# Performance work log

Measured on AMD Instinct MI355X. Metric: run time of the kernel, lower is better.

Reference implementation:

```python
import jax, jax.numpy as jnp
import numpy as np

K = 8          # kernels per group
H = 32         # groups (g // divisor)
NUM_DIL = 14   # int(log2((75000-1)/8)) + 1


def _gconv1d(x, w, d, p):
    # x: (B, H, T), w: (H*K, 1, 9) grouped conv, dilation d, padding p
    return jax.lax.conv_general_dilated(
        x, w, window_strides=(1,), padding=[(p, p)], rhs_dilation=(d,),
        dimension_numbers=("NCH", "OIH", "NCH"), feature_group_count=H)


def setup_inputs() -> dict:
    key = jax.random.key(0)
    kX, kW, kI = jax.random.split(key, 3)
    X = jax.random.normal(kX, (4, 17, 75000), dtype=jnp.float32)
    W = jax.random.normal(kW, (NUM_DIL, 2, K * H, 1, 9), dtype=jnp.float32)
    W = W - W.mean(-1, keepdims=True)
    W = W / jnp.abs(W).sum(-1, keepdims=True)
    idx = jax.random.randint(kI, (NUM_DIL, 2, H, 8), 0, 17, dtype=jnp.int32)
    return {"X": X, "W": W, "idx": idx}


def reference(X, W, idx):
    B = X.shape[0]
    diff_X = jnp.diff(X, axis=-1)  # (B, C, T-1)
    bi = jnp.arange(B)[:, None, None]
    hi = jnp.arange(H)[None, :, None]
    outs = []
    for di in range(NUM_DIL):
        d = 2 ** di
        p = 4 * d  # (9-1)*d // 2
        for diff_i in range(2):
            src = X if diff_i == 0 else diff_X
            # channel gather + sum: (B, H, 8, T) -> (B, H, T)
            g = src[:, idx[di, diff_i]].sum(2)
            z = _gconv1d(g, W[di, diff_i], d, p)  # (B, H*K, L)
            z = z.reshape(B, H, K, -1)            # (B, H, K, L)
            max_v = z.max(2)                       # (B, H, L)
            max_i = z.argmax(2)
            min_i = z.argmin(2)
            count_max = jnp.zeros((B, H, K), z.dtype).at[bi, hi, max_i].add(max_v)
            count_min = jnp.zeros((B, H, K), z.dtype).at[bi, hi, min_i].add(1.0)
            outs.append(count_max)
            outs.append(count_min)
    return jnp.concatenate(outs, axis=1).reshape(B, -1)  # (B, 14336)
```

## Files before the change

kernel.cpp:

```cpp
#include <hip/hip_runtime.h>

typedef float F2 __attribute__((ext_vector_type(2)));

#define NB 4
#define NC 17
#define T0 75000
#define NH 32
#define NK 8

__global__ void diffK(const float* __restrict__ X, float* __restrict__ D) {
    int t = blockIdx.x * 256 + threadIdx.x;
    int row = blockIdx.y;
    if (t < T0) {
        size_t o = (size_t)row * T0 + t;
        D[o] = (t < T0 - 1) ? (X[o + 1] - X[o]) : 0.f;
    }
}

__device__ __forceinline__ float packK(float z, int k) {
    unsigned u = (__float_as_uint(z) & 0xFFFFFFF8u) | (unsigned)k;
    return __uint_as_float(u);
}

__device__ __forceinline__ void pkfma_lo(F2& z, F2 g, unsigned long long w) {
    asm("v_pk_fma_f32 %0, %1, %2, %0 op_sel:[0,0,0] op_sel_hi:[1,0,1]"
        : "+v"(z) : "v"(g), "s"(w));
}
__device__ __forceinline__ void pkfma_hi(F2& z, F2 g, unsigned long long w) {
    asm("v_pk_fma_f32 %0, %1, %2, %0 op_sel:[0,1,0] op_sel_hi:[1,1,1]"
        : "+v"(z) : "v"(g), "s"(w));
}

template <int C>
__device__ __forceinline__ void epi8(const F2* Z, float* accM, unsigned long long& cnt) {
    float p[8];
#pragma unroll
    for (int k = 0; k < 8; ++k) p[k] = packK(C ? Z[k].y : Z[k].x, k);
    float ma = fmaxf(fmaxf(p[0], p[1]), p[2]);
    float mb = fmaxf(fmaxf(p[3], p[4]), p[5]);
    float mc = fmaxf(fmaxf(p[6], p[7]), ma);
    float best = fmaxf(mb, mc);
    float na = fminf(fminf(p[0], p[1]), p[2]);
    float nb = fminf(fminf(p[3], p[4]), p[5]);
    float nc = fminf(fminf(p[6], p[7]), na);
    float worst = fminf(nb, nc);
    int biK = __float_as_uint(best) & 7;
    int wiK = __float_as_uint(worst) & 7;
#pragma unroll
    for (int k = 0; k < 8; ++k) accM[k] += (k == biK) ? best : 0.f;
    cnt += 1ull << (wiK << 3);
}

constexpr int TS = 1024;
constexpr int A_TILES = 74;
constexpr int A_BLOCKS_PER_G = 128 * A_TILES;
constexpr int A_GROUPS = 12;
constexpr int A_TOTAL_BLOCKS = A_GROUPS * A_BLOCKS_PER_G;

template <bool USE_D>
__global__ __launch_bounds__(256) void kernA(const float* __restrict__ X,
                                             const float* __restrict__ Dws,
                                             const float* __restrict__ Wt,
                                             const int* __restrict__ idx,
                                             float* __restrict__ out) {
    __shared__ float Sbuf[TS + 8 * 32 + 2];
    __shared__ float red[4][16];

    const int tid = threadIdx.x;
    const int bid = blockIdx.x;
    const int ga = bid / A_BLOCKS_PER_G;
    const int rem = bid - ga * A_BLOCKS_PER_G;
    const int b = rem & 3;
    const int z = rem >> 2;
    const int h = z & 31;
    const int tile = z >> 5;
    const int di = ga >> 1, diff = ga & 1;
    const int d = 1 << di;
    const int T = T0 - diff;
    const int t0 = tile * TS;
    const int span = TS + 8 * d;
    const int g0 = t0 - 4 * d;

    const int* ip = idx + (ga * NH + h) * 8;
    int offs[8];
#pragma unroll
    for (int i = 0; i < 8; ++i)
        offs[i] = __builtin_amdgcn_readfirstlane((b * NC + ip[i]) * T0);

    if (USE_D) {
        const float* base = diff ? Dws : X;
        for (int e = tid * 2; e < span; e += 512) {
            int u = g0 + e;
            F2 s = {0.f, 0.f};
            if (u >= 0 && u + 1 < T0) {
#pragma unroll
                for (int i = 0; i < 8; ++i) s += *(const F2*)(base + offs[i] + u);
            } else {
#pragma unroll
                for (int c = 0; c < 2; ++c) {
                    int uc = u + c;
                    float sc = 0.f;
                    if (uc >= 0 && uc < T0) {
#pragma unroll
                        for (int i = 0; i < 8; ++i) sc += base[offs[i] + uc];
                    }
                    s[c] = sc;
                }
            }
            if (e + 1 < span) *(F2*)(Sbuf + e) = s;
            else Sbuf[e] = s.x;
        }
    } else {
        for (int ls = tid; ls < span; ls += 256) {
            int u = g0 + ls;
            float s = 0.f;
            if (diff) {
                if (u >= 0 && u < T0 - 1) {
#pragma unroll
                    for (int i = 0; i < 8; ++i) s += X[offs[i] + u + 1] - X[offs[i] + u];
                }
            } else {
                if (u >= 0 && u < T0) {
#pragma unroll
                    for (int i = 0; i < 8; ++i) s += X[offs[i] + u];
                }
            }
            Sbuf[ls] = s;
        }
    }
    __syncthreads();

    const int wbase = __builtin_amdgcn_readfirstlane((ga * (NK * NH) + h * NK) * 9);
    const unsigned long long* wq64 = (const unsigned long long*)(Wt + wbase);
    unsigned long long wq[36];
#pragma unroll
    for (int i = 0; i < 36; ++i) wq[i] = wq64[i];

    float accM[8];
#pragma unroll
    for (int k = 0; k < 8; ++k) accM[k] = 0.f;
    unsigned long long cnt = 0;

#pragma unroll
    for (int it = 0; it < 2; ++it) {
        int p = tid + it * 256;
        int t = t0 + p;
        F2 Z[8];
#pragma unroll
        for (int k = 0; k < 8; ++k) Z[k] = (F2){0.f, 0.f};
#pragma unroll
        for (int j = 0; j < 9; ++j) {
            F2 g;
            g.x = Sbuf[p + j * d];
            g.y = Sbuf[p + 512 + j * d];
#pragma unroll
            for (int k = 0; k < 8; ++k) {
                const int wi = k * 9 + j;
                if (wi & 1) pkfma_hi(Z[k], g, wq[wi >> 1]);
                else        pkfma_lo(Z[k], g, wq[wi >> 1]);
            }
        }
        if (t < T)       epi8<0>(Z, accM, cnt);
        if (t + 512 < T) epi8<1>(Z, accM, cnt);
    }

    float accC[8];
#pragma unroll
    for (int k = 0; k < 8; ++k) accC[k] = (float)((unsigned)(cnt >> (k * 8)) & 255u);

#pragma unroll
    for (int k = 0; k < 8; ++k) {
#pragma unroll
        for (int sh = 1; sh < 64; sh <<= 1) {
            accM[k] += __shfl_xor(accM[k], sh, 64);
            accC[k] += __shfl_xor(accC[k], sh, 64);
        }
    }
    int wv = tid >> 6, lane = tid & 63;
    if (lane == 0) {
#pragma unroll
        for (int k = 0; k < 8; ++k) { red[wv][k] = accM[k]; red[wv][8 + k] = accC[k]; }
    }
    __syncthreads();
    if (tid < 16) {
        float v = red[0][tid] + red[1][tid] + red[2][tid] + red[3][tid];
        int which = tid >> 3;
        int k = tid & 7;
        int o = ga * 2 + which;
        atomicAdd(&out[(size_t)b * 14336 + (o * NH + h) * NK + k], v);
    }
}

struct BG2 { int base, segs2, di, diff; };
constexpr BG2 BGS2[16] = {
    {0,     640,  6, 0}, {320,   640,  6, 1},
    {640,   640,  7, 0}, {960,   640,  7, 1},
    {1280,  640,  8, 0}, {1600,  640,  8, 1},
    {1920,  768,  9, 0}, {2304,  768,  9, 1},
    {2688, 1024, 10, 0}, {3200, 1024, 10, 1},
    {3712, 1024, 11, 0}, {4224, 1024, 11, 1},
    {4736, 2048, 12, 0}, {5760, 2048, 12, 1},
    {6784, 4096, 13, 0}, {8832, 4096, 13, 1},
};
constexpr int B2_BLOCKS = 10880;

template <bool USE_D>
__device__ __forceinline__ F2 gather2(const float* __restrict__ base,
                                      const int* offs, int u, int diffF) {
    F2 s = {0.f, 0.f};
    if (u >= 0 && u + 1 < T0) {
        if (!USE_D && diffF) {
            float m0 = 0.f, m1 = 0.f, m2 = 0.f;
#pragma unroll
            for (int i = 0; i < 8; ++i) {
                m0 += base[offs[i] + u];
                m1 += base[offs[i] + u + 1];
                m2 += (u + 2 < T0) ? base[offs[i] + u + 2] : base[offs[i] + u + 1];
            }
            s.x = m1 - m0;
            s.y = (u + 2 < T0) ? (m2 - m1) : 0.f;
        } else {
#pragma unroll
            for (int i = 0; i < 8; ++i) s += *(const F2*)(base + offs[i] + u);
        }
    } else if (u + 1 >= 0 && u < T0) {
#pragma unroll
        for (int c = 0; c < 2; ++c) {
            int uc = u + c;
            float sc = 0.f;
            if (uc >= 0 && uc < T0) {
                if (!USE_D && diffF) {
                    if (uc < T0 - 1) {
#pragma unroll
                        for (int i = 0; i < 8; ++i)
                            sc += base[offs[i] + uc + 1] - base[offs[i] + uc];
                    }
                } else {
#pragma unroll
                    for (int i = 0; i < 8; ++i) sc += base[offs[i] + uc];
                }
            }
            s[c] = sc;
        }
    }
    return s;
}

template <bool USE_D>
__global__ __launch_bounds__(256, 4) void kernB2(const float* __restrict__ X,
                                                 const float* __restrict__ Dws,
                                                 const float* __restrict__ Wt,
                                                 const int* __restrict__ idx,
                                                 float* __restrict__ out) {
    const int tid = threadIdx.x;
    const int bid = blockIdx.x;

    int di = 6, diff = 0, gig = 0, combo = 0, sg = 0;
#pragma unroll
    for (int g = 0; g < 16; ++g) {
        const int s2 = BGS2[g].segs2;
        if (bid >= BGS2[g].base && bid < BGS2[g].base + 128 * s2 / 256) {
            gig = (bid - BGS2[g].base) * 256 + tid;
            combo = gig / s2;
            sg = gig - combo * s2;
            di = BGS2[g].di; diff = BGS2[g].diff;
        }
    }
    combo = __builtin_amdgcn_readfirstlane(combo);
    di    = __builtin_amdgcn_readfirstlane(di);
    diff  = __builtin_amdgcn_readfirstlane(diff);

    const int d = 1 << di;
    const int T = T0 - diff;
    const int Q = (T + d - 1) >> di;
    const int ga = di * 2 + diff;
    const int b = combo & 3;
    const int h = combo >> 2;

    const int p = sg & ((d >> 1) - 1);
    const int q0 = (sg >> (di - 1)) * 60;
    const int r = 2 * p;

    const int* ip = idx + (ga * NH + h) * 8;
    int offs[8];
#pragma unroll
    for (int i = 0; i < 8; ++i)
        offs[i] = __builtin_amdgcn_readfirstlane((b * NC + ip[i]) * T0);

    const int wbase = __builtin_amdgcn_readfirstlane((ga * (NK * NH) + h * NK) * 9);
    const unsigned long long* wq64 = (const unsigned long long*)(Wt + wbase);
    unsigned long long wq[36];
#pragma unroll
    for (int i = 0; i < 36; ++i) wq[i] = wq64[i];

    const float* base = (USE_D && diff) ? Dws : X;

    float accM[8];
#pragma unroll
    for (int k = 0; k < 8; ++k) accM[k] = 0.f;
    unsigned long long cnt = 0;

    const int t0 = r + q0 * d;
    F2 buf[12];
    {
        int u = t0 - 4 * d;
#pragma unroll
        for (int m = 0; m < 12; ++m) { buf[m] = gather2<USE_D>(base, offs, u, diff); u += d; }
    }

    for (int outer = 0; outer < 5; ++outer) {
        if (q0 + outer * 12 >= Q) break;
        const int tb = t0 + outer * 12 * d;
#pragma unroll
        for (int ii = 0; ii < 12; ++ii) {
            const int t = tb + ii * d;
            F2 Z[8];
#pragma unroll
            for (int k = 0; k < 8; ++k) Z[k] = (F2){0.f, 0.f};
#pragma unroll
            for (int j = 0; j < 9; ++j) {
                F2 g = buf[(ii + j) % 12];
#pragma unroll
                for (int k = 0; k < 8; ++k) {
                    const int wi = k * 9 + j;
                    if (wi & 1) pkfma_hi(Z[k], g, wq[wi >> 1]);
                    else        pkfma_lo(Z[k], g, wq[wi >> 1]);
                }
            }
            if (t < T)     epi8<0>(Z, accM, cnt);
            if (t + 1 < T) epi8<1>(Z, accM, cnt);
            buf[ii] = gather2<USE_D>(base, offs, t + 8 * d, diff);
        }
    }

    float accC[8];
#pragma unroll
    for (int k = 0; k < 8; ++k) accC[k] = (float)((unsigned)(cnt >> (k * 8)) & 255u);

#pragma unroll
    for (int k = 0; k < 8; ++k) {
#pragma unroll
        for (int sh = 1; sh < 64; sh <<= 1) {
            accM[k] += __shfl_xor(accM[k], sh, 64);
            accC[k] += __shfl_xor(accC[k], sh, 64);
        }
    }
    if ((tid & 63) == 0) {
        size_t bb = (size_t)b * 14336;
        int o = ga * 2;
#pragma unroll
        for (int k = 0; k < 8; ++k) {
            atomicAdd(&out[bb + (o * NH + h) * NK + k],       accM[k]);
            atomicAdd(&out[bb + ((o + 1) * NH + h) * NK + k], accC[k]);
        }
    }
}

__global__ void zeroK(float* __restrict__ out, int n) {
    int i = blockIdx.x * 256 + threadIdx.x;
    if (i < n) out[i] = 0.f;
}

extern "C" void kernel_launch(void* const* d_in, const int* in_sizes, int n_in,
                              void* d_out, int out_size, void* d_ws, size_t ws_size,
                              hipStream_t stream) {
    const float* X  = (const float*)d_in[0];
    const float* Wt = (const float*)d_in[1];
    const int*  idx = (const int*)d_in[2];
    float* out = (float*)d_out;
    float* Dws = (float*)d_ws;

    const size_t D_BYTES = (size_t)NB * NC * T0 * sizeof(float);
    const bool useD = ws_size >= D_BYTES;

    zeroK<<<(out_size + 255) / 256, 256, 0, stream>>>(out, out_size);
    if (useD) {
        dim3 dg((T0 + 255) / 256, NB * NC);
        diffK<<<dg, 256, 0, stream>>>(X, Dws);
        kernA<true><<<A_TOTAL_BLOCKS, 256, 0, stream>>>(X, Dws, Wt, idx, out);
        kernB2<true><<<B2_BLOCKS, 256, 0, stream>>>(X, Dws, Wt, idx, out);
    } else {
        kernA<false><<<A_TOTAL_BLOCKS, 256, 0, stream>>>(X, Dws, Wt, idx, out);
        kernB2<false><<<B2_BLOCKS, 256, 0, stream>>>(X, Dws, Wt, idx, out);
    }
}
```

Measured before the change: 1.161 ms.

## Double kernA tile size, start conv with multiply, and reduce via shared memory

```diff
diff --git a/kernel.cpp b/kernel.cpp
--- a/kernel.cpp
+++ b/kernel.cpp
@@ -29,6 +29,14 @@
 __device__ __forceinline__ void pkfma_hi(F2& z, F2 g, unsigned long long w) {
     asm("v_pk_fma_f32 %0, %1, %2, %0 op_sel:[0,1,0] op_sel_hi:[1,1,1]"
         : "+v"(z) : "v"(g), "s"(w));
+}
+__device__ __forceinline__ void pkmul_lo(F2& z, F2 g, unsigned long long w) {
+    asm("v_pk_mul_f32 %0, %1, %2 op_sel:[0,0] op_sel_hi:[1,0]"
+        : "=v"(z) : "v"(g), "s"(w));
+}
+__device__ __forceinline__ void pkmul_hi(F2& z, F2 g, unsigned long long w) {
+    asm("v_pk_mul_f32 %0, %1, %2 op_sel:[0,1] op_sel_hi:[1,1]"
+        : "=v"(z) : "v"(g), "s"(w));
 }
 
 template <int C>
@@ -51,8 +59,26 @@
     cnt += 1ull << (wiK << 3);
 }
 
-constexpr int TS = 1024;
-constexpr int A_TILES = 74;
+__device__ __forceinline__ void conv9(F2* Z, const F2* g9, const unsigned long long* wq) {
+#pragma unroll
+    for (int k = 0; k < 8; ++k) {
+        const int wi = k * 9;
+        if (wi & 1) pkmul_hi(Z[k], g9[0], wq[wi >> 1]);
+        else        pkmul_lo(Z[k], g9[0], wq[wi >> 1]);
+    }
+#pragma unroll
+    for (int j = 1; j < 9; ++j) {
+#pragma unroll
+        for (int k = 0; k < 8; ++k) {
+            const int wi = k * 9 + j;
+            if (wi & 1) pkfma_hi(Z[k], g9[j], wq[wi >> 1]);
+            else        pkfma_lo(Z[k], g9[j], wq[wi >> 1]);
+        }
+    }
+}
+
+constexpr int TS = 2048;
+constexpr int A_TILES = 37;
 constexpr int A_BLOCKS_PER_G = 128 * A_TILES;
 constexpr int A_GROUPS = 12;
 constexpr int A_TOTAL_BLOCKS = A_GROUPS * A_BLOCKS_PER_G;
@@ -63,7 +89,7 @@
                                              const float* __restrict__ Wt,
                                              const int* __restrict__ idx,
                                              float* __restrict__ out) {
-    __shared__ float Sbuf[TS + 8 * 32 + 2];
+    __shared__ float Sbuf[16 * 257];
     __shared__ float red[4][16];
 
     const int tid = threadIdx.x;
@@ -142,44 +168,42 @@
     unsigned long long cnt = 0;
 
 #pragma unroll
-    for (int it = 0; it < 2; ++it) {
+    for (int it = 0; it < 4; ++it) {
         int p = tid + it * 256;
         int t = t0 + p;
+        F2 g9[9];
+#pragma unroll
+        for (int j = 0; j < 9; ++j) {
+            g9[j].x = Sbuf[p + j * d];
+            g9[j].y = Sbuf[p + 1024 + j * d];
+        }
         F2 Z[8];
-#pragma unroll
-        for (int k = 0; k < 8; ++k) Z[k] = (F2){0.f, 0.f};
-#pragma unroll
-        for (int j = 0; j < 9; ++j) {
-            F2 g;
-            g.x = Sbuf[p + j * d];
-            g.y = Sbuf[p + 512 + j * d];
-#pragma unroll
-            for (int k = 0; k < 8; ++k) {
-                const int wi = k * 9 + j;
-                if (wi & 1) pkfma_hi(Z[k], g, wq[wi >> 1]);
-                else        pkfma_lo(Z[k], g, wq[wi >> 1]);
-            }
-        }
-        if (t < T)       epi8<0>(Z, accM, cnt);
-        if (t + 512 < T) epi8<1>(Z, accM, cnt);
+        conv9(Z, g9, wq);
+        if (t < T)        epi8<0>(Z, accM, cnt);
+        if (t + 1024 < T) epi8<1>(Z, accM, cnt);
     }
 
     float accC[8];
 #pragma unroll
     for (int k = 0; k < 8; ++k) accC[k] = (float)((unsigned)(cnt >> (k * 8)) & 255u);
 
+    __syncthreads();
 #pragma unroll
     for (int k = 0; k < 8; ++k) {
-#pragma unroll
-        for (int sh = 1; sh < 64; sh <<= 1) {
-            accM[k] += __shfl_xor(accM[k], sh, 64);
-            accC[k] += __shfl_xor(accC[k], sh, 64);
-        }
-    }
-    int wv = tid >> 6, lane = tid & 63;
-    if (lane == 0) {
-#pragma unroll
-        for (int k = 0; k < 8; ++k) { red[wv][k] = accM[k]; red[wv][8 + k] = accC[k]; }
+        Sbuf[k * 257 + tid] = accM[k];
+        Sbuf[(k + 8) * 257 + tid] = accC[k];
+    }
+    __syncthreads();
+    {
+        int k = tid & 15, seg = tid >> 4;
+        const float* rp = Sbuf + k * 257 + seg * 16;
+        float s = 0.f;
+#pragma unroll
+        for (int i = 0; i < 16; ++i) s += rp[i];
+        s += __shfl_xor(s, 16, 64);
+        s += __shfl_xor(s, 32, 64);
+        int wv = tid >> 6;
+        if ((tid & 63) < 16) red[wv][k] = s;
     }
     __syncthreads();
     if (tid < 16) {
@@ -314,19 +338,11 @@
 #pragma unroll
         for (int ii = 0; ii < 12; ++ii) {
             const int t = tb + ii * d;
+            F2 g9[9];
+#pragma unroll
+            for (int j = 0; j < 9; ++j) g9[j] = buf[(ii + j) % 12];
             F2 Z[8];
-#pragma unroll
-            for (int k = 0; k < 8; ++k) Z[k] = (F2){0.f, 0.f};
-#pragma unroll
-            for (int j = 0; j < 9; ++j) {
-                F2 g = buf[(ii + j) % 12];
-#pragma unroll
-                for (int k = 0; k < 8; ++k) {
-                    const int wi = k * 9 + j;
-                    if (wi & 1) pkfma_hi(Z[k], g, wq[wi >> 1]);
-                    else        pkfma_lo(Z[k], g, wq[wi >> 1]);
-                }
-            }
+            conv9(Z, g9, wq);
             if (t < T)     epi8<0>(Z, accM, cnt);
             if (t + 1 < T) epi8<1>(Z, accM, cnt);
             buf[ii] = gather2<USE_D>(base, offs, t + 8 * d, diff);
```

Measured after the change: 939.9 us (median of 2 runs). 1.23x faster.
